# Performance work log

Measured on AMD Instinct MI355X. Metric: run time of the kernel, lower is better.

## Reference

```python
import jax, jax.numpy as jnp
import numpy as np


def _lstm_dir(x, W_ih, W_hh, b_ih, b_hh, reverse):
    # x: [T, B, Din] -> hs: [T, B, H]; PyTorch gate order i,f,g,o
    xs = x[::-1] if reverse else x
    gx = xs @ W_ih.T + (b_ih + b_hh)  # [T, B, 4H] precomputed input contribution
    H = W_hh.shape[1]
    B = x.shape[1]

    def step(carry, g):
        h, c = carry
        g = g + h @ W_hh.T
        i, f, gg, o = jnp.split(g, 4, axis=-1)
        c = jax.nn.sigmoid(f) * c + jax.nn.sigmoid(i) * jnp.tanh(gg)
        h = jax.nn.sigmoid(o) * jnp.tanh(c)
        return (h, c), h

    z = jnp.zeros((B, H), x.dtype)
    _, hs = jax.lax.scan(step, (z, z), gx)
    return hs[::-1] if reverse else hs


def _emissions(inputs, emb, layers, W_out, b_out):
    x = jnp.swapaxes(emb[inputs], 0, 1)  # [T, B, E]
    for (Wif, Whf, bif, bhf, Wib, Whb, bib, bhb) in layers:
        hf = _lstm_dir(x, Wif, Whf, bif, bhf, False)
        hb = _lstm_dir(x, Wib, Whb, bib, bhb, True)
        x = jnp.concatenate([hf, hb], axis=-1)  # [T, B, 2H]
    return x @ W_out.T + b_out  # [T, B, K]


def _viterbi(em, start_trans, end_trans, trans):
    # em: [T, B, K] -> (tags [B, T] int32, best_score [B])
    score0 = start_trans + em[0]  # [B, K]

    def fwd_step(score, e):
        s = score[:, :, None] + trans[None, :, :]  # [B, Kprev, Knext]
        bp = jnp.argmax(s, axis=1)
        return jnp.max(s, axis=1) + e, bp

    score, bps = jax.lax.scan(fwd_step, score0, em[1:])  # bps: [T-1, B, K]
    score = score + end_trans
    last_tag = jnp.argmax(score, axis=1)  # [B]
    best_score = jnp.max(score, axis=1)   # [B]

    def back_step(tag, bp):
        prev = jnp.take_along_axis(bp, tag[:, None], axis=1)[:, 0]
        return prev, prev

    _, prevs = jax.lax.scan(back_step, last_tag, bps, reverse=True)  # [T-1, B]
    tags = jnp.concatenate([prevs, last_tag[None]], axis=0)  # [T, B]
    return jnp.swapaxes(tags, 0, 1).astype(jnp.int32), best_score


def setup_inputs() -> dict:
    key = jax.random.key(0)
    ks = jax.random.split(key, 24)
    B, T, V, E, H, K = 64, 512, 30000, 256, 256, 32

    def n(k, shape, s=0.05):
        return jax.random.normal(k, shape, dtype=jnp.float32) * s

    d = {"inputs": jax.random.randint(ks[0], (B, T), 0, V)}
    d["emb"] = n(ks[1], (V, E), 0.1).at[0].set(0.0)  # padding_idx=0
    i = 2
    for l, din in [(0, E), (1, 2 * H)]:
        for dr in ("f", "b"):
            d[f"W_ih_l{l}_{dr}"] = n(ks[i], (4 * H, din)); i += 1
            d[f"W_hh_l{l}_{dr}"] = n(ks[i], (4 * H, H)); i += 1
            d[f"b_ih_l{l}_{dr}"] = n(ks[i], (4 * H,)); i += 1
            d[f"b_hh_l{l}_{dr}"] = n(ks[i], (4 * H,)); i += 1
    d["W_out"] = n(ks[i], (K, 2 * H)); i += 1
    d["b_out"] = n(ks[i], (K,)); i += 1
    d["start_trans"] = n(ks[i], (K,)); i += 1
    d["end_trans"] = n(ks[i], (K,)); i += 1
    d["trans"] = n(ks[i], (K, K)); i += 1
    return d


def reference(inputs, emb,
              W_ih_l0_f, W_hh_l0_f, b_ih_l0_f, b_hh_l0_f,
              W_ih_l0_b, W_hh_l0_b, b_ih_l0_b, b_hh_l0_b,
              W_ih_l1_f, W_hh_l1_f, b_ih_l1_f, b_hh_l1_f,
              W_ih_l1_b, W_hh_l1_b, b_ih_l1_b, b_hh_l1_b,
              W_out, b_out, start_trans, end_trans, trans):
    layers = [
        (W_ih_l0_f, W_hh_l0_f, b_ih_l0_f, b_hh_l0_f,
         W_ih_l0_b, W_hh_l0_b, b_ih_l0_b, b_hh_l0_b),
        (W_ih_l1_f, W_hh_l1_f, b_ih_l1_f, b_hh_l1_f,
         W_ih_l1_b, W_hh_l1_b, b_ih_l1_b, b_hh_l1_b),
    ]
    em = _emissions(inputs, emb, layers, W_out, b_out)
    tags, _ = _viterbi(em, start_trans, end_trans, trans)
    return tags  # [B, T] best tag sequence per batch element
```

## Files before the change

### kernel.cpp

```cpp
#include <hip/hip_runtime.h>
#include <math.h>
#include <stdint.h>

#define TLEN 512
#define BSZ  64
#define EDIM 256
#define HDIM 256
#define GDIM 1024
#define KTAG 32

__device__ __forceinline__ float sigf(float x) { return 1.0f / (1.0f + expf(-x)); }

template<int KDIM, bool GATHER, bool TOXBUF>
__global__ __launch_bounds__(512, 2)
void lstm_fused(
    const float* __restrict__ gx_f, const float* __restrict__ gx_b,
    const float* __restrict__ Wf, const float* __restrict__ Wb,
    float* __restrict__ xout, float* __restrict__ hbuf,
    float* __restrict__ state, uint64_t* __restrict__ hxs,
    unsigned int fbase,
    int t0f, int t0b, int C, int init, int nlstm, int nmt,
    const float* __restrict__ A, const int* __restrict__ idx,
    const float* __restrict__ Bf, const float* __restrict__ Bb,
    const float* __restrict__ b1f, const float* __restrict__ b2f,
    const float* __restrict__ b1b, const float* __restrict__ b2b,
    float* __restrict__ ogx_f, float* __restrict__ ogx_b,
    int gt0f, int gt0b, int gr0f, int gr0b)
{
    __shared__ __align__(16) float h_lds[2][256];
    __shared__ __align__(16) float ps[2][2][256];
    __shared__ __align__(16) float gxs[2][256];
    __shared__ __align__(16) float As[8][132];
    __shared__ __align__(16) float Bs[8][132];

    const int bid = blockIdx.x;
    const int t = threadIdx.x;

    if (bid < nlstm) {
        const int cl  = bid & 63;
        const int rb  = bid >> 6;
        const int dir = cl >> 5;
        const int b0g = (cl & 31) * 2;
        const float* gx = dir ? gx_b : gx_f;
        const float* W  = dir ? Wb : Wf;
        const int t0 = dir ? t0b : t0f;

        const int rr = t & 255;
        const int kh = t >> 8;
        const int urow = ((rr >> 6) * 256) + rb * 64 + (rr & 63);

        float4 w[32];
        {
            const float4* wrow = (const float4*)(W + (size_t)urow * HDIM + kh * 128);
            #pragma unroll
            for (int i = 0; i < 32; ++i) w[i] = wrow[i];
        }
        #pragma unroll
        for (int i = 0; i < 32; ++i)
            asm volatile("" : "+v"(w[i].x), "+v"(w[i].y), "+v"(w[i].z), "+v"(w[i].w));

        float cc = 0.0f;
        for (int i = t; i < 2 * 256; i += 512) {
            int b = i >> 8, u = i & 255;
            h_lds[b][u] = init ? 0.0f
                : state[(((size_t)dir * BSZ + (b0g + b)) * 2) * HDIM + u];
        }
        if (t < 128) {
            int b = t >> 6, ug = rb * 64 + (t & 63);
            if (!init)
                cc = state[(((size_t)dir * BSZ + (b0g + b)) * 2) * HDIM + HDIM + ug];
        }
        __syncthreads();
        __builtin_amdgcn_s_setprio(1);

        const int pb = t >> 8;
        {
            const int tl0 = dir ? (C - 1) : 0;
        }
        float gv = gx[((size_t)(dir ? (C - 1) : 0) * BSZ + (b0g + pb)) * GDIM + urow];

        for (int s = 0; s < C; ++s) {
            const int tloc = dir ? (C - 1 - s) : s;
            float a0 = 0.f, a1 = 0.f;
            #pragma unroll
            for (int i = 0; i < 32; ++i) {
                float4 h0 = *(const float4*)&h_lds[0][kh * 128 + i * 4];
                float4 h1 = *(const float4*)&h_lds[1][kh * 128 + i * 4];
                a0 = fmaf(w[i].x, h0.x, a0); a0 = fmaf(w[i].y, h0.y, a0);
                a0 = fmaf(w[i].z, h0.z, a0); a0 = fmaf(w[i].w, h0.w, a0);
                a1 = fmaf(w[i].x, h1.x, a1); a1 = fmaf(w[i].y, h1.y, a1);
                a1 = fmaf(w[i].z, h1.z, a1); a1 = fmaf(w[i].w, h1.w, a1);
            }
            ps[kh][0][rr] = a0; ps[kh][1][rr] = a1;
            gxs[pb][rr] = gv;
            __syncthreads();
            const unsigned want = fbase + (unsigned)(s + 1);
            if (t < 128) {
                const int b = t >> 6, ul = t & 63;
                float pi = ps[0][b][ul]       + ps[1][b][ul]       + gxs[b][ul];
                float pf = ps[0][b][64 + ul]  + ps[1][b][64 + ul]  + gxs[b][64 + ul];
                float pg = ps[0][b][128 + ul] + ps[1][b][128 + ul] + gxs[b][128 + ul];
                float po = ps[0][b][192 + ul] + ps[1][b][192 + ul] + gxs[b][192 + ul];
                float iv = sigf(pi), fv = sigf(pf), gv2 = tanhf(pg), ov = sigf(po);
                cc = fv * cc + iv * gv2;
                float hv = ov * tanhf(cc);
                const int ug = rb * 64 + ul;
                h_lds[b][ug] = hv;
                uint64_t pv = ((uint64_t)want << 32) | (uint64_t)__float_as_uint(hv);
                __hip_atomic_store(&hxs[(((size_t)(s & 1) * 64 + cl) * 2 + b) * 256 + ug],
                                   pv, __ATOMIC_RELAXED, __HIP_MEMORY_SCOPE_AGENT);
                if (TOXBUF)
                    xout[((size_t)(t0 + tloc) * BSZ + (b0g + b)) * 512 + dir * HDIM + ug] = hv;
                else
                    hbuf[(((size_t)dir * C + tloc) * BSZ + (b0g + b)) * HDIM + ug] = hv;
            }
            if (s + 1 < C) {
                const int tl2 = dir ? (C - 2 - s) : (s + 1);
                gv = gx[((size_t)tl2 * BSZ + (b0g + pb)) * GDIM + urow];
            }
            __builtin_amdgcn_s_setprio(0);
            if (t < 384) {
                const int b = t / 192;
                const int ix = t % 192;
                const int u = (ix < rb * 64) ? ix : ix + 64;
                const uint64_t* src =
                    &hxs[(((size_t)(s & 1) * 64 + cl) * 2 + b) * 256 + u];
                uint64_t v;
                do {
                    v = __hip_atomic_load(src, __ATOMIC_RELAXED,
                                          __HIP_MEMORY_SCOPE_AGENT);
                } while ((unsigned)(v >> 32) != want);
                h_lds[b][u] = __uint_as_float((unsigned)v);
            }
            __builtin_amdgcn_s_setprio(1);
            __syncthreads();
        }
        __builtin_amdgcn_s_setprio(0);
        if (t < 128) {
            int b = t >> 6, ug = rb * 64 + (t & 63);
            size_t sb = (((size_t)dir * BSZ + (b0g + b)) * 2) * HDIM;
            state[sb + ug] = h_lds[b][ug];
            state[sb + HDIM + ug] = cc;
        }
        return;
    }

    const int g = bid - nlstm;
    const int mx = g % nmt;
    const int ny = g / nmt;
    const int mt = mx * 128;
    const int ngc = ny * 128;
    const bool isF = (ngc < GDIM);
    const int nt = isF ? ngc : (ngc - GDIM);
    const float* Bw = isF ? Bf : Bb;
    const float* bias1 = isF ? b1f : b1b;
    const float* bias2 = isF ? b2f : b2b;
    float* Cc = isF ? ogx_f : ogx_b;
    const int t0 = isF ? gt0f : gt0b;
    const int r0 = isF ? gr0f : gr0b;

    const int tx = t & 15;
    const int ty = t >> 4;
    const int l_row = t >> 2;
    const int l_k = (t & 3) * 2;

    const float* arow;
    if (GATHER) {
        int m = mt + l_row;
        int tt = t0 + (m >> 6);
        int b = m & 63;
        arow = A + (size_t)idx[b * TLEN + tt] * (size_t)KDIM;
    } else {
        arow = A + (size_t)(r0 + mt + l_row) * (size_t)KDIM;
    }
    const float* brow = Bw + (size_t)(nt + l_row) * (size_t)KDIM;

    float acc[4][8];
    #pragma unroll
    for (int i = 0; i < 4; ++i)
        #pragma unroll
        for (int j = 0; j < 8; ++j) acc[i][j] = 0.0f;

    float2 av = *(const float2*)(arow + l_k);
    float2 bv = *(const float2*)(brow + l_k);
    for (int k0 = 0; k0 < KDIM; k0 += 8) {
        __syncthreads();
        As[l_k + 0][l_row] = av.x; As[l_k + 1][l_row] = av.y;
        Bs[l_k + 0][l_row] = bv.x; Bs[l_k + 1][l_row] = bv.y;
        __syncthreads();
        if (k0 + 8 < KDIM) {
            av = *(const float2*)(arow + k0 + 8 + l_k);
            bv = *(const float2*)(brow + k0 + 8 + l_k);
        }
        #pragma unroll
        for (int k = 0; k < 8; ++k) {
            float a[4], bb2[8];
            *(float4*)(a)       = *(const float4*)&As[k][ty * 4];
            *(float4*)(bb2)     = *(const float4*)&Bs[k][tx * 4];
            *(float4*)(bb2 + 4) = *(const float4*)&Bs[k][64 + tx * 4];
            #pragma unroll
            for (int i = 0; i < 4; ++i)
                #pragma unroll
                for (int j = 0; j < 8; ++j)
                    acc[i][j] = fmaf(a[i], bb2[j], acc[i][j]);
        }
    }

    float bs[8];
    #pragma unroll
    for (int j = 0; j < 4; ++j) bs[j] = bias1[nt + tx * 4 + j] + bias2[nt + tx * 4 + j];
    #pragma unroll
    for (int j = 4; j < 8; ++j) bs[j] = bias1[nt + 64 + tx * 4 + j - 4] + bias2[nt + 64 + tx * 4 + j - 4];
    #pragma unroll
    for (int i = 0; i < 4; ++i) {
        size_t row = (size_t)(mt + ty * 4 + i);
        float* cp0 = Cc + row * GDIM + nt + tx * 4;
        float* cp1 = Cc + row * GDIM + nt + 64 + tx * 4;
        *(float4*)cp0 = make_float4(acc[i][0] + bs[0], acc[i][1] + bs[1],
                                    acc[i][2] + bs[2], acc[i][3] + bs[3]);
        *(float4*)cp1 = make_float4(acc[i][4] + bs[4], acc[i][5] + bs[5],
                                    acc[i][6] + bs[6], acc[i][7] + bs[7]);
    }
}

__global__ __launch_bounds__(256)
void emis_part(const float* __restrict__ hbuf, const float* __restrict__ Wo,
               float* __restrict__ em_f, float* __restrict__ em_b,
               int t0f, int t0b, int C)
{
    __shared__ float Ws[128][33];
    const int dir = blockIdx.y;
    const int tid = threadIdx.x;
    const int r = tid >> 5;
    const int kk = tid & 31;
    const int mloc = blockIdx.x * 8 + r;
    const float* hrow = hbuf + ((size_t)dir * C * BSZ + mloc) * HDIM;
    float* emo = dir ? em_b : em_f;
    const int t0 = dir ? t0b : t0f;
    float acc = 0.0f;
    for (int kc = 0; kc < HDIM; kc += 128) {
        __syncthreads();
        for (int i = tid; i < KTAG * 128; i += 256) {
            int wk = i >> 7;
            int k = i & 127;
            Ws[k][wk] = Wo[(size_t)wk * 512 + dir * HDIM + kc + k];
        }
        __syncthreads();
        #pragma unroll 8
        for (int k4 = 0; k4 < 32; ++k4) {
            float4 xv = *(const float4*)(hrow + kc + k4 * 4);
            acc = fmaf(xv.x, Ws[k4 * 4 + 0][kk], acc);
            acc = fmaf(xv.y, Ws[k4 * 4 + 1][kk], acc);
            acc = fmaf(xv.z, Ws[k4 * 4 + 2][kk], acc);
            acc = fmaf(xv.w, Ws[k4 * 4 + 3][kk], acc);
        }
    }
    const int tloc = mloc >> 6;
    const int b = mloc & 63;
    emo[(((size_t)(t0 + tloc)) * BSZ + b) * KTAG + kk] = acc;
}

__global__ __launch_bounds__(64)
void viterbi(const float* __restrict__ em_f, const float* __restrict__ em_b,
             const float* __restrict__ bo,
             const float* __restrict__ st, const float* __restrict__ en,
             const float* __restrict__ tr, int* __restrict__ out)
{
    const int b = blockIdx.x;
    const int lane = threadIdx.x;
    __shared__ float s_tr[KTAG][KTAG + 1];
    __shared__ float s_sc[KTAG];
    __shared__ float s_fin[KTAG];
    __shared__ unsigned char s_bp[TLEN - 1][KTAG];
    for (int i = lane; i < KTAG * KTAG; i += 64)
        s_tr[i >> 5][i & 31] = tr[i];
    float eFn = 0.f, eBn = 0.f;
    if (lane < KTAG) {
        size_t e0 = (size_t)b * KTAG + lane;
        s_sc[lane] = st[lane] + em_f[e0] + em_b[e0] + bo[lane];
        size_t e1 = ((size_t)1 * BSZ + b) * KTAG + lane;
        eFn = em_f[e1]; eBn = em_b[e1];
    }
    __syncthreads();
    for (int t = 1; t < TLEN; ++t) {
        float ecF = eFn, ecB = eBn;
        if (t + 1 < TLEN && lane < KTAG) {
            size_t e2 = ((size_t)(t + 1) * BSZ + b) * KTAG + lane;
            eFn = em_f[e2]; eBn = em_b[e2];
        }
        float best = -3.0e38f;
        int arg = 0;
        if (lane < KTAG) {
            #pragma unroll
            for (int i = 0; i < KTAG; ++i) {
                float c = s_sc[i] + s_tr[i][lane];
                if (c > best) { best = c; arg = i; }
            }
        }
        __syncthreads();
        if (lane < KTAG) {
            s_sc[lane] = best + ecF + ecB + bo[lane];
            s_bp[t - 1][lane] = (unsigned char)arg;
        }
        __syncthreads();
    }
    if (lane < KTAG) s_fin[lane] = s_sc[lane] + en[lane];
    __syncthreads();
    if (lane == 0) {
        int tag = 0;
        float bv = s_fin[0];
        for (int i = 1; i < KTAG; ++i)
            if (s_fin[i] > bv) { bv = s_fin[i]; tag = i; }
        out[(size_t)b * TLEN + (TLEN - 1)] = tag;
        for (int t = TLEN - 2; t >= 0; --t) {
            tag = s_bp[t][tag];
            out[(size_t)b * TLEN + t] = tag;
        }
    }
}

extern "C" void kernel_launch(void* const* d_in, const int* in_sizes, int n_in,
                              void* d_out, int out_size, void* d_ws, size_t ws_size,
                              hipStream_t stream)
{
    (void)in_sizes; (void)n_in; (void)out_size;
    const int*   inputs     = (const int*)d_in[0];
    const float* emb        = (const float*)d_in[1];
    const float* W_ih_l0_f  = (const float*)d_in[2];
    const float* W_hh_l0_f  = (const float*)d_in[3];
    const float* b_ih_l0_f  = (const float*)d_in[4];
    const float* b_hh_l0_f  = (const float*)d_in[5];
    const float* W_ih_l0_b  = (const float*)d_in[6];
    const float* W_hh_l0_b  = (const float*)d_in[7];
    const float* b_ih_l0_b  = (const float*)d_in[8];
    const float* b_hh_l0_b  = (const float*)d_in[9];
    const float* W_ih_l1_f  = (const float*)d_in[10];
    const float* W_hh_l1_f  = (const float*)d_in[11];
    const float* b_ih_l1_f  = (const float*)d_in[12];
    const float* b_hh_l1_f  = (const float*)d_in[13];
    const float* W_ih_l1_b  = (const float*)d_in[14];
    const float* W_hh_l1_b  = (const float*)d_in[15];
    const float* b_ih_l1_b  = (const float*)d_in[16];
    const float* b_hh_l1_b  = (const float*)d_in[17];
    const float* W_out      = (const float*)d_in[18];
    const float* b_out      = (const float*)d_in[19];
    const float* start_tr   = (const float*)d_in[20];
    const float* end_tr     = (const float*)d_in[21];
    const float* trans      = (const float*)d_in[22];

    const size_t XBUF = 67108864ull;
    const size_t PERC = 4ull * 262144 + 131072;
    const size_t TAIL = 2ull * 4194304 + 524288 + 524288;
    int C = 8;
    for (int cand = TLEN; cand >= 8; cand >>= 1) {
        if (XBUF + (size_t)cand * PERC + TAIL <= ws_size) { C = cand; break; }
    }
    char* ws = (char*)d_ws;
    float* xbuf  = (float*)(ws);
    char*  p     = ws + XBUF;
    float* gxA_f = (float*)(p); p += (size_t)C * 262144;
    float* gxA_b = (float*)(p); p += (size_t)C * 262144;
    float* gxB_f = (float*)(p); p += (size_t)C * 262144;
    float* gxB_b = (float*)(p); p += (size_t)C * 262144;
    float* hbuf  = (float*)(p); p += (size_t)C * 131072;
    float* em_f  = (float*)(p); p += 4194304;
    float* em_b  = (float*)(p); p += 4194304;
    float* state = (float*)(p); p += 524288;
    uint64_t* hxs = (uint64_t*)(p);
    int* outi = (int*)d_out;

    const int nc = TLEN / C;
    const int nmt = C / 2;
    const int NG = nmt * 16;
    const int NL = 256;
    float* gxf[2] = { gxA_f, gxB_f };
    float* gxb[2] = { gxA_b, gxB_b };

    hipMemsetAsync(hxs, 0, 524288, stream);
    unsigned fbase = 0;

    lstm_fused<EDIM, true, true><<<NG, 512, 0, stream>>>(
        gxA_f, gxA_b, W_hh_l0_f, W_hh_l0_b, xbuf, nullptr, state, hxs, 0,
        0, 0, C, 1, 0, nmt,
        emb, inputs, W_ih_l0_f, W_ih_l0_b,
        b_ih_l0_f, b_hh_l0_f, b_ih_l0_b, b_hh_l0_b,
        gxA_f, gxA_b, 0, TLEN - C, 0, 0);
    for (int c = 0; c < nc; ++c) {
        int cur = c & 1, nxt = cur ^ 1;
        int hasN = (c + 1 < nc);
        int t0f = c * C, t0b = TLEN - (c + 1) * C;
        int g0f = (c + 1) * C, g0b = TLEN - (c + 2) * C;
        lstm_fused<EDIM, true, true><<<NL + (hasN ? NG : 0), 512, 0, stream>>>(
            gxf[cur], gxb[cur], W_hh_l0_f, W_hh_l0_b, xbuf, nullptr, state,
            hxs, fbase, t0f, t0b, C, c == 0 ? 1 : 0, NL, nmt,
            emb, inputs, W_ih_l0_f, W_ih_l0_b,
            b_ih_l0_f, b_hh_l0_f, b_ih_l0_b, b_hh_l0_b,
            gxf[nxt], gxb[nxt], g0f, g0b, 0, 0);
        fbase += (unsigned)C;
    }
    lstm_fused<512, false, false><<<NG, 512, 0, stream>>>(
        gxA_f, gxA_b, W_hh_l1_f, W_hh_l1_b, nullptr, hbuf, state, hxs, 0,
        0, 0, C, 1, 0, nmt,
        xbuf, nullptr, W_ih_l1_f, W_ih_l1_b,
        b_ih_l1_f, b_hh_l1_f, b_ih_l1_b, b_hh_l1_b,
        gxA_f, gxA_b, 0, TLEN - C, 0, (TLEN - C) * BSZ);
    for (int c = 0; c < nc; ++c) {
        int cur = c & 1, nxt = cur ^ 1;
        int hasN = (c + 1 < nc);
        int t0f = c * C, t0b = TLEN - (c + 1) * C;
        int g0f = (c + 1) * C, g0b = TLEN - (c + 2) * C;
        lstm_fused<512, false, false><<<NL + (hasN ? NG : 0), 512, 0, stream>>>(
            gxf[cur], gxb[cur], W_hh_l1_f, W_hh_l1_b, nullptr, hbuf, state,
            hxs, fbase, t0f, t0b, C, c == 0 ? 1 : 0, NL, nmt,
            xbuf, nullptr, W_ih_l1_f, W_ih_l1_b,
            b_ih_l1_f, b_hh_l1_f, b_ih_l1_b, b_hh_l1_b,
            gxf[nxt], gxb[nxt], g0f, g0b, g0f * BSZ, g0b * BSZ);
        fbase += (unsigned)C;
        dim3 ge(C * 8, 2);
        emis_part<<<ge, 256, 0, stream>>>(hbuf, W_out, em_f, em_b, t0f, t0b, C);
    }

    viterbi<<<64, 64, 0, stream>>>(em_f, em_b, b_out, start_tr, end_tr, trans,
                                   outi);
}
```

Baseline: 4.247 ms.

## Restructure recurrent LSTM blocks to 8 batches each, streaming transposed W_hh from cache

Each recurrent block now handles 8 batch rows instead of 2, which cuts the recurrent block count from 256 to 64 and reduces the number of peers exchanging hidden state through the global flag buffer. W_hh is no longer held in registers. It is pre-transposed into a float4-interleaved layout by a new kernel and re-read from global memory/L2 on every timestep, so loads are coalesced. The intent is to trade register-resident weights for higher per-block arithmetic reuse and fewer, larger synchronisation groups. The cost is per-step weight memory traffic, higher LDS use, and launch bounds relaxed to one block per CU.

```diff
diff --git a/kernel.cpp b/kernel.cpp
--- a/kernel.cpp
+++ b/kernel.cpp
@@ -11,11 +11,21 @@
 
 __device__ __forceinline__ float sigf(float x) { return 1.0f / (1.0f + expf(-x)); }
 
+__global__ __launch_bounds__(256)
+void transpose_w(const float* __restrict__ W, float4* __restrict__ Wt)
+{
+    const int t = threadIdx.x;
+    const int j = blockIdx.x * 4 + (t >> 6);
+    const int l = t & 63;
+    float4 v = *(const float4*)(W + (size_t)j * HDIM + l * 4);
+    Wt[(size_t)l * GDIM + j] = v;
+}
+
 template<int KDIM, bool GATHER, bool TOXBUF>
-__global__ __launch_bounds__(512, 2)
+__global__ __launch_bounds__(512, 1)
 void lstm_fused(
     const float* __restrict__ gx_f, const float* __restrict__ gx_b,
-    const float* __restrict__ Wf, const float* __restrict__ Wb,
+    const float4* __restrict__ Wt_f, const float4* __restrict__ Wt_b,
     float* __restrict__ xout, float* __restrict__ hbuf,
     float* __restrict__ state, uint64_t* __restrict__ hxs,
     unsigned int fbase,
@@ -27,9 +37,9 @@
     float* __restrict__ ogx_f, float* __restrict__ ogx_b,
     int gt0f, int gt0b, int gr0f, int gr0b)
 {
-    __shared__ __align__(16) float h_lds[2][256];
-    __shared__ __align__(16) float ps[2][2][256];
-    __shared__ __align__(16) float gxs[2][256];
+    __shared__ __align__(16) float h_lds[8][256];
+    __shared__ __align__(16) float ps[2][8][256];
+    __shared__ __align__(16) float gxs[8][256];
     __shared__ __align__(16) float As[8][132];
     __shared__ __align__(16) float Bs[8][132];
 
@@ -37,35 +47,26 @@
     const int t = threadIdx.x;
 
     if (bid < nlstm) {
-        const int cl  = bid & 63;
-        const int rb  = bid >> 6;
-        const int dir = cl >> 5;
-        const int b0g = (cl & 31) * 2;
+        const int cl  = bid & 15;
+        const int rb  = bid >> 4;
+        const int dir = cl >> 3;
+        const int b0g = (cl & 7) * 8;
         const float* gx = dir ? gx_b : gx_f;
-        const float* W  = dir ? Wb : Wf;
+        const float4* Wt = dir ? Wt_b : Wt_f;
         const int t0 = dir ? t0b : t0f;
 
         const int rr = t & 255;
         const int kh = t >> 8;
         const int urow = ((rr >> 6) * 256) + rb * 64 + (rr & 63);
-
-        float4 w[32];
-        {
-            const float4* wrow = (const float4*)(W + (size_t)urow * HDIM + kh * 128);
-            #pragma unroll
-            for (int i = 0; i < 32; ++i) w[i] = wrow[i];
-        }
-        #pragma unroll
-        for (int i = 0; i < 32; ++i)
-            asm volatile("" : "+v"(w[i].x), "+v"(w[i].y), "+v"(w[i].z), "+v"(w[i].w));
+        const float4* Wp = Wt + (size_t)(kh * 32) * GDIM + urow;
 
         float cc = 0.0f;
-        for (int i = t; i < 2 * 256; i += 512) {
+        for (int i = t; i < 8 * 256; i += 512) {
             int b = i >> 8, u = i & 255;
             h_lds[b][u] = init ? 0.0f
                 : state[(((size_t)dir * BSZ + (b0g + b)) * 2) * HDIM + u];
         }
-        if (t < 128) {
+        {
             int b = t >> 6, ug = rb * 64 + (t & 63);
             if (!init)
                 cc = state[(((size_t)dir * BSZ + (b0g + b)) * 2) * HDIM + HDIM + ug];
@@ -73,41 +74,69 @@
         __syncthreads();
         __builtin_amdgcn_s_setprio(1);
 
-        const int pb = t >> 8;
+        float gv0, gv1, gv2, gv3;
         {
             const int tl0 = dir ? (C - 1) : 0;
-        }
-        float gv = gx[((size_t)(dir ? (C - 1) : 0) * BSZ + (b0g + pb)) * GDIM + urow];
+            const float* g0 = gx + (size_t)tl0 * BSZ * GDIM + urow;
+            gv0 = g0[(size_t)(b0g + kh * 4 + 0) * GDIM];
+            gv1 = g0[(size_t)(b0g + kh * 4 + 1) * GDIM];
+            gv2 = g0[(size_t)(b0g + kh * 4 + 2) * GDIM];
+            gv3 = g0[(size_t)(b0g + kh * 4 + 3) * GDIM];
+        }
 
         for (int s = 0; s < C; ++s) {
             const int tloc = dir ? (C - 1 - s) : s;
-            float a0 = 0.f, a1 = 0.f;
+            float a0 = 0.f, a1 = 0.f, a2 = 0.f, a3 = 0.f;
+            float a4 = 0.f, a5 = 0.f, a6 = 0.f, a7 = 0.f;
             #pragma unroll
             for (int i = 0; i < 32; ++i) {
+                float4 wv = Wp[(size_t)i * GDIM];
                 float4 h0 = *(const float4*)&h_lds[0][kh * 128 + i * 4];
                 float4 h1 = *(const float4*)&h_lds[1][kh * 128 + i * 4];
-                a0 = fmaf(w[i].x, h0.x, a0); a0 = fmaf(w[i].y, h0.y, a0);
-                a0 = fmaf(w[i].z, h0.z, a0); a0 = fmaf(w[i].w, h0.w, a0);
-                a1 = fmaf(w[i].x, h1.x, a1); a1 = fmaf(w[i].y, h1.y, a1);
-                a1 = fmaf(w[i].z, h1.z, a1); a1 = fmaf(w[i].w, h1.w, a1);
+                float4 h2 = *(const float4*)&h_lds[2][kh * 128 + i * 4];
+                float4 h3 = *(const float4*)&h_lds[3][kh * 128 + i * 4];
+                float4 h4 = *(const float4*)&h_lds[4][kh * 128 + i * 4];
+                float4 h5 = *(const float4*)&h_lds[5][kh * 128 + i * 4];
+                float4 h6 = *(const float4*)&h_lds[6][kh * 128 + i * 4];
+                float4 h7 = *(const float4*)&h_lds[7][kh * 128 + i * 4];
+                a0 = fmaf(wv.x, h0.x, a0); a0 = fmaf(wv.y, h0.y, a0);
+                a0 = fmaf(wv.z, h0.z, a0); a0 = fmaf(wv.w, h0.w, a0);
+                a1 = fmaf(wv.x, h1.x, a1); a1 = fmaf(wv.y, h1.y, a1);
+                a1 = fmaf(wv.z, h1.z, a1); a1 = fmaf(wv.w, h1.w, a1);
+                a2 = fmaf(wv.x, h2.x, a2); a2 = fmaf(wv.y, h2.y, a2);
+                a2 = fmaf(wv.z, h2.z, a2); a2 = fmaf(wv.w, h2.w, a2);
+                a3 = fmaf(wv.x, h3.x, a3); a3 = fmaf(wv.y, h3.y, a3);
+                a3 = fmaf(wv.z, h3.z, a3); a3 = fmaf(wv.w, h3.w, a3);
+                a4 = fmaf(wv.x, h4.x, a4); a4 = fmaf(wv.y, h4.y, a4);
+                a4 = fmaf(wv.z, h4.z, a4); a4 = fmaf(wv.w, h4.w, a4);
+                a5 = fmaf(wv.x, h5.x, a5); a5 = fmaf(wv.y, h5.y, a5);
+                a5 = fmaf(wv.z, h5.z, a5); a5 = fmaf(wv.w, h5.w, a5);
+                a6 = fmaf(wv.x, h6.x, a6); a6 = fmaf(wv.y, h6.y, a6);
+                a6 = fmaf(wv.z, h6.z, a6); a6 = fmaf(wv.w, h6.w, a6);
+                a7 = fmaf(wv.x, h7.x, a7); a7 = fmaf(wv.y, h7.y, a7);
+                a7 = fmaf(wv.z, h7.z, a7); a7 = fmaf(wv.w, h7.w, a7);
             }
             ps[kh][0][rr] = a0; ps[kh][1][rr] = a1;
-            gxs[pb][rr] = gv;
+            ps[kh][2][rr] = a2; ps[kh][3][rr] = a3;
+            ps[kh][4][rr] = a4; ps[kh][5][rr] = a5;
+            ps[kh][6][rr] = a6; ps[kh][7][rr] = a7;
+            gxs[kh * 4 + 0][rr] = gv0; gxs[kh * 4 + 1][rr] = gv1;
+            gxs[kh * 4 + 2][rr] = gv2; gxs[kh * 4 + 3][rr] = gv3;
             __syncthreads();
             const unsigned want = fbase + (unsigned)(s + 1);
-            if (t < 128) {
+            {
                 const int b = t >> 6, ul = t & 63;
                 float pi = ps[0][b][ul]       + ps[1][b][ul]       + gxs[b][ul];
                 float pf = ps[0][b][64 + ul]  + ps[1][b][64 + ul]  + gxs[b][64 + ul];
                 float pg = ps[0][b][128 + ul] + ps[1][b][128 + ul] + gxs[b][128 + ul];
                 float po = ps[0][b][192 + ul] + ps[1][b][192 + ul] + gxs[b][192 + ul];
-                float iv = sigf(pi), fv = sigf(pf), gv2 = tanhf(pg), ov = sigf(po);
-                cc = fv * cc + iv * gv2;
+                float iv = sigf(pi), fv = sigf(pf), gv2_ = tanhf(pg), ov = sigf(po);
+                cc = fv * cc + iv * gv2_;
                 float hv = ov * tanhf(cc);
                 const int ug = rb * 64 + ul;
                 h_lds[b][ug] = hv;
                 uint64_t pv = ((uint64_t)want << 32) | (uint64_t)__float_as_uint(hv);
-                __hip_atomic_store(&hxs[(((size_t)(s & 1) * 64 + cl) * 2 + b) * 256 + ug],
+                __hip_atomic_store(&hxs[(((size_t)(s & 1) * 16 + cl) * 8 + b) * 256 + ug],
                                    pv, __ATOMIC_RELAXED, __HIP_MEMORY_SCOPE_AGENT);
                 if (TOXBUF)
                     xout[((size_t)(t0 + tloc) * BSZ + (b0g + b)) * 512 + dir * HDIM + ug] = hv;
@@ -116,15 +145,21 @@
             }
             if (s + 1 < C) {
                 const int tl2 = dir ? (C - 2 - s) : (s + 1);
-                gv = gx[((size_t)tl2 * BSZ + (b0g + pb)) * GDIM + urow];
+                const float* g2 = gx + (size_t)tl2 * BSZ * GDIM + urow;
+                gv0 = g2[(size_t)(b0g + kh * 4 + 0) * GDIM];
+                gv1 = g2[(size_t)(b0g + kh * 4 + 1) * GDIM];
+                gv2 = g2[(size_t)(b0g + kh * 4 + 2) * GDIM];
+                gv3 = g2[(size_t)(b0g + kh * 4 + 3) * GDIM];
             }
             __builtin_amdgcn_s_setprio(0);
-            if (t < 384) {
-                const int b = t / 192;
-                const int ix = t % 192;
-                const int u = (ix < rb * 64) ? ix : ix + 64;
+            #pragma unroll
+            for (int q = 0; q < 3; ++q) {
+                int i = t + q * 512;
+                int b = i / 192;
+                int ix = i % 192;
+                int u = (ix < rb * 64) ? ix : ix + 64;
                 const uint64_t* src =
-                    &hxs[(((size_t)(s & 1) * 64 + cl) * 2 + b) * 256 + u];
+                    &hxs[(((size_t)(s & 1) * 16 + cl) * 8 + b) * 256 + u];
                 uint64_t v;
                 do {
                     v = __hip_atomic_load(src, __ATOMIC_RELAXED,
@@ -136,7 +171,7 @@
             __syncthreads();
         }
         __builtin_amdgcn_s_setprio(0);
-        if (t < 128) {
+        {
             int b = t >> 6, ug = rb * 64 + (t & 63);
             size_t sb = (((size_t)dir * BSZ + (b0g + b)) * 2) * HDIM;
             state[sb + ug] = h_lds[b][ug];
@@ -350,7 +385,7 @@
 
     const size_t XBUF = 67108864ull;
     const size_t PERC = 4ull * 262144 + 131072;
-    const size_t TAIL = 2ull * 4194304 + 524288 + 524288;
+    const size_t TAIL = 2ull * 4194304 + 524288 + 524288 + 2097152;
     int C = 8;
     for (int cand = TLEN; cand >= 8; cand >>= 1) {
         if (XBUF + (size_t)cand * PERC + TAIL <= ws_size) { C = cand; break; }
@@ -366,21 +401,25 @@
     float* em_f  = (float*)(p); p += 4194304;
     float* em_b  = (float*)(p); p += 4194304;
     float* state = (float*)(p); p += 524288;
-    uint64_t* hxs = (uint64_t*)(p);
+    uint64_t* hxs = (uint64_t*)(p); p += 524288;
+    float4* wt_f = (float4*)(p); p += 1048576;
+    float4* wt_b = (float4*)(p);
     int* outi = (int*)d_out;
 
     const int nc = TLEN / C;
     const int nmt = C / 2;
     const int NG = nmt * 16;
-    const int NL = 256;
+    const int NL = 64;
     float* gxf[2] = { gxA_f, gxB_f };
     float* gxb[2] = { gxA_b, gxB_b };
 
     hipMemsetAsync(hxs, 0, 524288, stream);
     unsigned fbase = 0;
 
+    transpose_w<<<256, 256, 0, stream>>>(W_hh_l0_f, wt_f);
+    transpose_w<<<256, 256, 0, stream>>>(W_hh_l0_b, wt_b);
     lstm_fused<EDIM, true, true><<<NG, 512, 0, stream>>>(
-        gxA_f, gxA_b, W_hh_l0_f, W_hh_l0_b, xbuf, nullptr, state, hxs, 0,
+        gxA_f, gxA_b, wt_f, wt_b, xbuf, nullptr, state, hxs, 0,
         0, 0, C, 1, 0, nmt,
         emb, inputs, W_ih_l0_f, W_ih_l0_b,
         b_ih_l0_f, b_hh_l0_f, b_ih_l0_b, b_hh_l0_b,
@@ -391,15 +430,17 @@
         int t0f = c * C, t0b = TLEN - (c + 1) * C;
         int g0f = (c + 1) * C, g0b = TLEN - (c + 2) * C;
         lstm_fused<EDIM, true, true><<<NL + (hasN ? NG : 0), 512, 0, stream>>>(
-            gxf[cur], gxb[cur], W_hh_l0_f, W_hh_l0_b, xbuf, nullptr, state,
+            gxf[cur], gxb[cur], wt_f, wt_b, xbuf, nullptr, state,
             hxs, fbase, t0f, t0b, C, c == 0 ? 1 : 0, NL, nmt,
             emb, inputs, W_ih_l0_f, W_ih_l0_b,
             b_ih_l0_f, b_hh_l0_f, b_ih_l0_b, b_hh_l0_b,
             gxf[nxt], gxb[nxt], g0f, g0b, 0, 0);
         fbase += (unsigned)C;
     }
+    transpose_w<<<256, 256, 0, stream>>>(W_hh_l1_f, wt_f);
+    transpose_w<<<256, 256, 0, stream>>>(W_hh_l1_b, wt_b);
     lstm_fused<512, false, false><<<NG, 512, 0, stream>>>(
-        gxA_f, gxA_b, W_hh_l1_f, W_hh_l1_b, nullptr, hbuf, state, hxs, 0,
+        gxA_f, gxA_b, wt_f, wt_b, nullptr, hbuf, state, hxs, 0,
         0, 0, C, 1, 0, nmt,
         xbuf, nullptr, W_ih_l1_f, W_ih_l1_b,
         b_ih_l1_f, b_hh_l1_f, b_ih_l1_b, b_hh_l1_b,
@@ -410,7 +451,7 @@
         int t0f = c * C, t0b = TLEN - (c + 1) * C;
         int g0f = (c + 1) * C, g0b = TLEN - (c + 2) * C;
         lstm_fused<512, false, false><<<NL + (hasN ? NG : 0), 512, 0, stream>>>(
-            gxf[cur], gxb[cur], W_hh_l1_f, W_hh_l1_b, nullptr, hbuf, state,
+            gxf[cur], gxb[cur], wt_f, wt_b, nullptr, hbuf, state,
             hxs, fbase, t0f, t0b, C, c == 0 ? 1 : 0, NL, nmt,
             xbuf, nullptr, W_ih_l1_f, W_ih_l1_b,
             b_ih_l1_f, b_hh_l1_f, b_ih_l1_b, b_hh_l1_b,
```

Result: slower. 6.974 ms (+64.2%).
